# Kernel tuning notes

Measured on AMD Instinct MI355X. Metric: run time of the kernel, lower is better.

Reference implementation:

```python
import jax, jax.numpy as jnp
import numpy as np

B, S, HID = 1, 2048, 2048
NH, NKV, D = 32, 4, 128   # query heads, kv heads, head_dim
ROPE_THETA = 1e6
EPS = 1e-6


def _rms_norm(x, w):
    # per-head RMSNorm over head_dim, computed in fp32 (Qwen3MoeRMSNorm)
    xf = x.astype(jnp.float32)
    var = jnp.mean(xf * xf, axis=-1, keepdims=True)
    return (w * (xf * jax.lax.rsqrt(var + EPS))).astype(x.dtype)


def _rotate_half(x):
    x1, x2 = jnp.split(x, 2, axis=-1)
    return jnp.concatenate([-x2, x1], axis=-1)


def setup_inputs() -> dict:
    key = jax.random.key(0)
    ks = jax.random.split(key, 5)
    hidden_states = jax.random.normal(ks[0], (B, S, HID), jnp.float32)
    # weights stored as (in, out); torch Linear computes x @ W.T with W (out,in) -- same math
    wq = jax.random.normal(ks[1], (HID, NH * D), jnp.float32) * 0.02
    wk = jax.random.normal(ks[2], (HID, NKV * D), jnp.float32) * 0.02
    wv = jax.random.normal(ks[3], (HID, NKV * D), jnp.float32) * 0.02
    wo = jax.random.normal(ks[4], (NH * D, HID), jnp.float32) * 0.02
    q_norm_w = jnp.ones((D,), jnp.float32)
    k_norm_w = jnp.ones((D,), jnp.float32)
    # RoPE tables (rotate_half convention, like HF Qwen3)
    inv_freq = 1.0 / (ROPE_THETA ** (jnp.arange(0, D, 2, dtype=jnp.float32) / D))
    freqs = jnp.arange(S, dtype=jnp.float32)[:, None] * inv_freq[None, :]  # [S, D/2]
    emb = jnp.concatenate([freqs, freqs], axis=-1)  # [S, D]
    cos, sin = jnp.cos(emb), jnp.sin(emb)
    # causal mask (True = keep)
    attention_mask = jnp.tril(jnp.ones((S, S), bool))[None, None]
    return {
        'hidden_states': hidden_states, 'cos': cos, 'sin': sin,
        'wq': wq, 'wk': wk, 'wv': wv, 'wo': wo,
        'q_norm_w': q_norm_w, 'k_norm_w': k_norm_w,
        'attention_mask': attention_mask, 'start_pos': 0,
    }


def reference(hidden_states, cos, sin, wq, wk, wv, wo, q_norm_w, k_norm_w,
              attention_mask, start_pos):
    b, s, _ = hidden_states.shape
    # projections + per-head RMSNorm, then [B, H, S, D]
    q = _rms_norm((hidden_states @ wq).reshape(b, s, NH, D), q_norm_w).transpose(0, 2, 1, 3)
    k = _rms_norm((hidden_states @ wk).reshape(b, s, NKV, D), k_norm_w).transpose(0, 2, 1, 3)
    v = (hidden_states @ wv).reshape(b, s, NKV, D).transpose(0, 2, 1, 3)
    # rotary embedding (rotate_half form); start_pos=0 -> tables already aligned
    c = cos[None, None, :, :]
    sn = sin[None, None, :, :]
    q = q * c + _rotate_half(q) * sn
    k = k * c + _rotate_half(k) * sn
    # GQA: repeat kv heads to match query heads
    groups = NH // NKV
    k = jnp.repeat(k, groups, axis=1)
    v = jnp.repeat(v, groups, axis=1)
    scaling = D ** -0.5
    scores = jnp.einsum('bhqd,bhkd->bhqk', q, k) * scaling  # [B, NH, S, S]
    scores = jnp.where(attention_mask, scores, jnp.float32(-1e9))
    attn = jax.nn.softmax(scores, axis=-1)
    out = jnp.einsum('bhqk,bhkd->bhqd', attn, v)  # [B, NH, S, D]
    out = out.transpose(0, 2, 1, 3).reshape(b, s, NH * D)
    return out @ wo
```

## Files before the change

kernel.cpp:

```cpp
#include <hip/hip_runtime.h>
#include <hip/hip_bf16.h>

using short4v = __attribute__((ext_vector_type(4))) short;
using short8 = __attribute__((ext_vector_type(8))) short;
using f32x4  = __attribute__((ext_vector_type(4))) float;

#define SEQ 2048
#define NHEAD 32
#define NKVH 4
#define HDIM 128
#define QK_SCALE_LOG2 (0.08838834764831845f * 1.44269504088896340f)

__device__ __forceinline__ float fast_exp2(float x) { return __builtin_amdgcn_exp2f(x); }
__device__ __forceinline__ float b2f(short u) {
    return __uint_as_float(((unsigned)(unsigned short)u) << 16);
}
__device__ __forceinline__ short f2bb(float f) {
    __hip_bfloat16 h = __float2bfloat16(f);
    return *reinterpret_cast<short*>(&h);
}

__global__ __launch_bounds__(256) void prep_kernel(
    const float* __restrict__ hs, __hip_bfloat16* __restrict__ hsb,
    const float* __restrict__ wq, const float* __restrict__ wk, const float* __restrict__ wv,
    const float* __restrict__ wo,
    __hip_bfloat16* __restrict__ WqkvT, __hip_bfloat16* __restrict__ WoT) {
    const int b = blockIdx.x, tid = threadIdx.x;
    if (b < 4096) {
        int i = b * 256 + tid;
        float4 v = ((const float4*)hs)[i];
        __hip_bfloat16 h4[4] = {__float2bfloat16(v.x), __float2bfloat16(v.y),
                                __float2bfloat16(v.z), __float2bfloat16(v.w)};
        ((ushort4*)hsb)[i] = *(ushort4*)h4;
        return;
    }
    __shared__ float tile[32][33];
    const float* W; __hip_bfloat16* Wt; int N, ld, nb, kb;
    if (b < 12288)      { int bb = b - 4096;  W = wq; Wt = WqkvT;                       N = 4096; ld = 2048; nb = (bb & 127) * 32; kb = (bb >> 7) * 32; }
    else if (b < 13312) { int bb = b - 12288; W = wk; Wt = WqkvT + (size_t)4096 * 2048; N = 512;  ld = 2048; nb = (bb & 15) * 32;  kb = (bb >> 4) * 32; }
    else if (b < 14336) { int bb = b - 13312; W = wv; Wt = WqkvT + (size_t)4608 * 2048; N = 512;  ld = 2048; nb = (bb & 15) * 32;  kb = (bb >> 4) * 32; }
    else                { int bb = b - 14336; W = wo; Wt = WoT;                         N = 2048; ld = 4096; nb = (bb & 63) * 32;  kb = (bb >> 6) * 32; }
    int tx = tid & 31, ty = tid >> 5;
    for (int j = 0; j < 32; j += 8)
        tile[ty + j][tx] = W[(size_t)(kb + ty + j) * N + nb + tx];
    __syncthreads();
    for (int j = 0; j < 32; j += 8)
        Wt[(size_t)(nb + ty + j) * ld + kb + tx] = __float2bfloat16(tile[tx][ty + j]);
}

__global__ void add3b_kernel(const __hip_bfloat16* __restrict__ a, const __hip_bfloat16* __restrict__ b,
                             const __hip_bfloat16* __restrict__ c, float* __restrict__ o, int n4) {
    int i = blockIdx.x * blockDim.x + threadIdx.x;
    if (i >= n4) return;
    short4v x = ((const short4v*)a)[i];
    short4v y = ((const short4v*)b)[i];
    short4v z = ((const short4v*)c)[i];
    float4 r = {b2f(x[0]) + b2f(y[0]) + b2f(z[0]), b2f(x[1]) + b2f(y[1]) + b2f(z[1]),
                b2f(x[2]) + b2f(y[2]) + b2f(z[2]), b2f(x[3]) + b2f(y[3]) + b2f(z[3])};
    ((float4*)o)[i] = r;
}

#define BM 128
#define BN 128
#define BKK 32
template <typename OutT>
__global__ __launch_bounds__(256) void gemm_bt_kernel(
    const __hip_bfloat16* __restrict__ A, const __hip_bfloat16* __restrict__ Bt,
    OutT* __restrict__ C, int M, int N, int KextMax, int ld, int koff, long long czstride, int Ktot) {
    const int kstart = blockIdx.z * koff;
    const int Kext = min(KextMax, Ktot - kstart);
    A  += (size_t)kstart;
    Bt += (size_t)kstart;
    C  += (size_t)blockIdx.z * czstride;
    __shared__ __align__(16) __hip_bfloat16 sA[BM * BKK];
    __shared__ __align__(16) __hip_bfloat16 sB[BN * BKK];
    const int tid = threadIdx.x;
    const int w = tid >> 6, l = tid & 63;
    const int wr = w >> 1, wc = w & 1;
    const int row0 = blockIdx.y * BM;
    const int col0 = blockIdx.x * BN;
    const int srow = l >> 2;
    const int scol = (l & 3) * 8;

    f32x4 acc[4][4] = {};
    const int fr = l & 15;
    const int fc = (l >> 4) * 8;

    for (int k0 = 0; k0 < Kext; k0 += BKK) {
        for (int i = 0; i < 2; ++i) {
            int c = i * 4 + w;
            const __hip_bfloat16* ga = A + (size_t)(row0 + c * 16 + srow) * ld + k0 + scol;
            __builtin_amdgcn_global_load_lds((const __attribute__((address_space(1))) void*)ga,
                                             (__attribute__((address_space(3))) void*)&sA[c * 16 * BKK], 16, 0, 0);
            const __hip_bfloat16* gb = Bt + (size_t)(col0 + c * 16 + srow) * ld + k0 + scol;
            __builtin_amdgcn_global_load_lds((const __attribute__((address_space(1))) void*)gb,
                                             (__attribute__((address_space(3))) void*)&sB[c * 16 * BKK], 16, 0, 0);
        }
        __syncthreads();
        short8 af[4], bfr[4];
        for (int m = 0; m < 4; ++m)
            af[m] = *(const short8*)&sA[(wr * 64 + m * 16 + fr) * BKK + fc];
        for (int n = 0; n < 4; ++n)
            bfr[n] = *(const short8*)&sB[(wc * 64 + n * 16 + fr) * BKK + fc];
        for (int m = 0; m < 4; ++m)
            for (int n = 0; n < 4; ++n)
                acc[m][n] = __builtin_amdgcn_mfma_f32_16x16x32_bf16(af[m], bfr[n], acc[m][n], 0, 0, 0);
        __syncthreads();
    }
    const int fq = l >> 4;
    for (int m = 0; m < 4; ++m)
        for (int n = 0; n < 4; ++n)
            for (int r = 0; r < 4; ++r) {
                int row = row0 + wr * 64 + m * 16 + fq * 4 + r;
                int col = col0 + wc * 64 + n * 16 + fr;
                float v = acc[m][n][r];
                if constexpr (__is_same(OutT, float)) C[(size_t)row * N + col] = v;
                else C[(size_t)row * N + col] = __float2bfloat16(v);
            }
}

__global__ __launch_bounds__(256) void pack_kernel(
    const __hip_bfloat16* __restrict__ P0, const __hip_bfloat16* __restrict__ P1,
    const float* __restrict__ cosp, const float* __restrict__ sinp,
    const float* __restrict__ qnw, const float* __restrict__ knw,
    __hip_bfloat16* __restrict__ Qh, __hip_bfloat16* __restrict__ Kh, __hip_bfloat16* __restrict__ Vt) {
    const int tid = threadIdx.x;
    const int rloc = tid >> 4, l16 = tid & 15;
    const int r = blockIdx.y * 16 + rloc;
    const int s = blockIdx.x * 2 + (r >= 40 ? 1 : 0);
    const int slot = (r >= 40) ? r - 40 : r;
    int off;
    if (slot < 32)      off = slot * 128;
    else if (slot < 36) off = 4096 + (slot - 32) * 128;
    else                off = 4608 + (slot - 36) * 128;
    const int d0 = l16 * 4;
    const size_t base = (size_t)s * 5120 + off;

    short4v a0 = *(const short4v*)&P0[base + d0];
    short4v a1 = *(const short4v*)&P0[base + d0 + 64];
    short4v b0 = *(const short4v*)&P1[base + d0];
    short4v b1 = *(const short4v*)&P1[base + d0 + 64];
    float x1[4], x2[4];
    for (int j = 0; j < 4; ++j) {
        x1[j] = b2f(a0[j]) + b2f(b0[j]);
        x2[j] = b2f(a1[j]) + b2f(b1[j]);
    }

    if (slot >= 36) {
        int t = slot - 36;
        for (int j = 0; j < 4; ++j) {
            Vt[((size_t)t * 128 + d0 + j) * SEQ + s]      = __float2bfloat16(x1[j]);
            Vt[((size_t)t * 128 + d0 + 64 + j) * SEQ + s] = __float2bfloat16(x2[j]);
        }
        return;
    }
    float ss = 0.f;
    for (int j = 0; j < 4; ++j) ss += x1[j] * x1[j] + x2[j] * x2[j];
    for (int x = 1; x < 16; x <<= 1) ss += __shfl_xor(ss, x);
    float rs = rsqrtf(ss * (1.0f / 128.0f) + 1e-6f);

    f32x4 c4 = *(const f32x4*)&cosp[(size_t)s * 128 + d0];
    f32x4 s4 = *(const f32x4*)&sinp[(size_t)s * 128 + d0];
    const float* wgt = (slot < 32) ? qnw : knw;
    f32x4 w1 = *(const f32x4*)&wgt[d0];
    f32x4 w2 = *(const f32x4*)&wgt[d0 + 64];
    const float scl = (slot < 32) ? QK_SCALE_LOG2 : 1.0f;

    short4v o1, o2;
    for (int j = 0; j < 4; ++j) {
        float a = x1[j] * rs * w1[j], b = x2[j] * rs * w2[j];
        o1[j] = f2bb((a * c4[j] - b * s4[j]) * scl);
        o2[j] = f2bb((b * c4[j] + a * s4[j]) * scl);
    }
    __hip_bfloat16* dst;
    if (slot < 32) dst = Qh + ((size_t)slot * SEQ + s) * 128;
    else           dst = Kh + ((size_t)(slot - 32) * SEQ + s) * 128;
    *(short4v*)&dst[d0]      = o1;
    *(short4v*)&dst[d0 + 64] = o2;
}

__global__ __launch_bounds__(256, 2) void attn_kernel(
    const __hip_bfloat16* __restrict__ Qh,
    const __hip_bfloat16* __restrict__ Kh,
    const __hip_bfloat16* __restrict__ Vt,
    __hip_bfloat16* __restrict__ Oa) {
    __shared__ __align__(16) __hip_bfloat16 sK[2][64 * 128];
    __shared__ __align__(16) __hip_bfloat16 sV[2][128 * 64];
    __shared__ __align__(16) __hip_bfloat16 sP[4][16 * 72];

    const int tid = threadIdx.x;
    const int w = tid >> 6, l = tid & 63;
    const int bx = blockIdx.x;
    const int y = bx & 7;
    const int qtA = bx >> 3;
    const int qbaseA = qtA * 16;
    const int qbaseB = (127 - qtA) * 16;
    const int hkv = y >> 1;
    const int h = y * 4 + w;
    const int fr = l & 15, g = l >> 4;

    const __hip_bfloat16* Kp = Kh + (size_t)hkv * SEQ * HDIM;
    const __hip_bfloat16* Vp = Vt + (size_t)hkv * HDIM * SEQ;
    __hip_bfloat16* myP = &sP[w][0];

    short8 qfA[4], qfB[4];
    {
        const __hip_bfloat16* QpA = Qh + ((size_t)h * SEQ + qbaseA) * HDIM;
        const __hip_bfloat16* QpB = Qh + ((size_t)h * SEQ + qbaseB) * HDIM;
        for (int c = 0; c < 4; ++c) {
            qfA[c] = *(const short8*)&QpA[fr * HDIM + c * 32 + g * 8];
            qfB[c] = *(const short8*)&QpB[fr * HDIM + c * 32 + g * 8];
        }
    }

    f32x4 oaccA[8] = {}, oaccB[8] = {};
    float mrowA[4], lpartA[4], mrowB[4], lpartB[4];
    for (int r = 0; r < 4; ++r) {
        mrowA[r] = -3.0e38f; lpartA[r] = 0.f;
        mrowB[r] = -3.0e38f; lpartB[r] = 0.f;
    }

    const int xr = (fr & 7) << 4;
    const int nA = ((qbaseA + 15) >> 6) + 1;
    const int nB = ((qbaseB + 15) >> 6) + 1;

    auto stage = [&](int buf, int kbase) {
        for (int i = 0; i < 4; ++i) {
            int blk = i * 4 + w;
            {
                int row = blk * 4 + (l >> 4);
                int cb = ((l & 15) * 16) ^ ((row & 7) << 4);
                const __hip_bfloat16* src = Kp + (size_t)(kbase + row) * HDIM + (cb >> 1);
                __builtin_amdgcn_global_load_lds((const __attribute__((address_space(1))) void*)src,
                    (__attribute__((address_space(3))) void*)&sK[buf][blk * 512], 16, 0, 0);
            }
            {
                int row = blk * 8 + (l >> 3);
                int cb = ((l & 7) * 16) ^ ((row & 7) << 4);
                const __hip_bfloat16* src = Vp + (size_t)row * SEQ + kbase + (cb >> 1);
                __builtin_amdgcn_global_load_lds((const __attribute__((address_space(1))) void*)src,
                    (__attribute__((address_space(3))) void*)&sV[buf][blk * 512], 16, 0, 0);
            }
        }
    };

#define PROCESS(QF, OACC, MROW, LPART, QBASE)                                          \
    {                                                                                  \
        f32x4 s[4] = {};                                                               \
        __builtin_amdgcn_s_setprio(1);                                                 \
        for (int j = 0; j < 4; ++j) {                                                  \
            const __hip_bfloat16* kp = &sK[buf][(j * 16 + fr) * 128];                  \
            for (int c = 0; c < 4; ++c) {                                              \
                short8 kf = *(const short8*)&kp[((c * 64 + g * 16) ^ xr) >> 1];        \
                s[j] = __builtin_amdgcn_mfma_f32_16x16x32_bf16(QF[c], kf, s[j], 0, 0, 0); \
            }                                                                          \
        }                                                                              \
        __builtin_amdgcn_s_setprio(0);                                                 \
        float v[4][4], mloc[4];                                                        \
        const bool full = (kbase + 63 <= (QBASE));                                     \
        for (int r = 0; r < 4; ++r) {                                                  \
            if (full) {                                                                \
                v[r][0] = s[0][r]; v[r][1] = s[1][r]; v[r][2] = s[2][r]; v[r][3] = s[3][r]; \
            } else {                                                                   \
                const int qg = (QBASE) + g * 4 + r;                                    \
                v[r][0] = (kbase + fr      <= qg) ? s[0][r] : -1e30f;                  \
                v[r][1] = (kbase + 16 + fr <= qg) ? s[1][r] : -1e30f;                  \
                v[r][2] = (kbase + 32 + fr <= qg) ? s[2][r] : -1e30f;                  \
                v[r][3] = (kbase + 48 + fr <= qg) ? s[3][r] : -1e30f;                  \
            }                                                                          \
            float m = fmaxf(fmaxf(v[r][0], v[r][1]), fmaxf(v[r][2], v[r][3]));         \
            for (int x = 1; x < 16; x <<= 1) m = fmaxf(m, __shfl_xor(m, x));           \
            mloc[r] = m;                                                               \
        }                                                                              \
        int grow = (mloc[0] > MROW[0] + 12.0f) | (mloc[1] > MROW[1] + 12.0f) |         \
                   (mloc[2] > MROW[2] + 12.0f) | (mloc[3] > MROW[3] + 12.0f);          \
        if (__any(grow)) {                                                             \
            for (int r = 0; r < 4; ++r) {                                              \
                float mnew = fmaxf(MROW[r], mloc[r]);                                  \
                float corr = fast_exp2(MROW[r] - mnew);                                \
                MROW[r] = mnew;                                                        \
                LPART[r] *= corr;                                                      \
                for (int dt = 0; dt < 8; ++dt) OACC[dt][r] *= corr;                    \
            }                                                                          \
        }                                                                              \
        for (int r = 0; r < 4; ++r) {                                                  \
            float e0 = fast_exp2(v[r][0] - MROW[r]);                                   \
            float e1 = fast_exp2(v[r][1] - MROW[r]);                                   \
            float e2 = fast_exp2(v[r][2] - MROW[r]);                                   \
            float e3 = fast_exp2(v[r][3] - MROW[r]);                                   \
            LPART[r] += (e0 + e1) + (e2 + e3);                                         \
            const int prow = (g * 4 + r) * 72;                                         \
            myP[prow + fr]      = __float2bfloat16(e0);                                \
            myP[prow + 16 + fr] = __float2bfloat16(e1);                                \
            myP[prow + 32 + fr] = __float2bfloat16(e2);                                \
            myP[prow + 48 + fr] = __float2bfloat16(e3);                                \
        }                                                                              \
        short8 pa0 = *(const short8*)&myP[fr * 72 + g * 8];                            \
        short8 pa1 = *(const short8*)&myP[fr * 72 + 32 + g * 8];                       \
        __builtin_amdgcn_s_setprio(1);                                                 \
        for (int dt = 0; dt < 8; ++dt) {                                               \
            const __hip_bfloat16* vp = &sV[buf][(dt * 16 + fr) * 64];                  \
            short8 vb0 = *(const short8*)&vp[((g * 16)      ^ xr) >> 1];               \
            short8 vb1 = *(const short8*)&vp[((g * 16 + 64) ^ xr) >> 1];               \
            OACC[dt] = __builtin_amdgcn_mfma_f32_16x16x32_bf16(pa0, vb0, OACC[dt], 0, 0, 0); \
            OACC[dt] = __builtin_amdgcn_mfma_f32_16x16x32_bf16(pa1, vb1, OACC[dt], 0, 0, 0); \
        }                                                                              \
        __builtin_amdgcn_s_setprio(0);                                                 \
    }

    stage(0, 0);
    __syncthreads();

    for (int t = 0; t < nB; ++t) {
        const int kbase = t * 64;
        const int buf = t & 1;
        if (t + 1 < nB) stage(buf ^ 1, kbase + 64);

        if (t < nA) PROCESS(qfA, oaccA, mrowA, lpartA, qbaseA);
        PROCESS(qfB, oaccB, mrowB, lpartB, qbaseB);

        __syncthreads();
    }
#undef PROCESS

    float invA[4], invB[4];
    for (int r = 0; r < 4; ++r) {
        float la = lpartA[r], lb = lpartB[r];
        for (int x = 1; x < 16; x <<= 1) { la += __shfl_xor(la, x); lb += __shfl_xor(lb, x); }
        invA[r] = 1.0f / la;
        invB[r] = 1.0f / lb;
    }
    for (int dt = 0; dt < 8; ++dt)
        for (int r = 0; r < 4; ++r) {
            int qgA = qbaseA + g * 4 + r;
            int qgB = qbaseB + g * 4 + r;
            Oa[(size_t)qgA * (NHEAD * HDIM) + h * HDIM + dt * 16 + fr] =
                __float2bfloat16(oaccA[dt][r] * invA[r]);
            Oa[(size_t)qgB * (NHEAD * HDIM) + h * HDIM + dt * 16 + fr] =
                __float2bfloat16(oaccB[dt][r] * invB[r]);
        }
}

extern "C" void kernel_launch(void* const* d_in, const int* in_sizes, int n_in,
                              void* d_out, int out_size, void* d_ws, size_t ws_size,
                              hipStream_t stream) {
    const float* hs   = (const float*)d_in[0];
    const float* cosp = (const float*)d_in[1];
    const float* sinp = (const float*)d_in[2];
    const float* wq   = (const float*)d_in[3];
    const float* wk   = (const float*)d_in[4];
    const float* wv   = (const float*)d_in[5];
    const float* wo   = (const float*)d_in[6];
    const float* qnw  = (const float*)d_in[7];
    const float* knw  = (const float*)d_in[8];
    float* out = (float*)d_out;
    char* ws = (char*)d_ws;

    __hip_bfloat16* hsb    = (__hip_bfloat16*)(ws);
    __hip_bfloat16* WqkvT  = (__hip_bfloat16*)(ws + 8388608);
    __hip_bfloat16* WoT    = (__hip_bfloat16*)(ws + 29360128);
    __hip_bfloat16* P0     = (__hip_bfloat16*)(ws + 46137344);
    __hip_bfloat16* P1     = (__hip_bfloat16*)(ws + 67108864);
    __hip_bfloat16* Qh     = (__hip_bfloat16*)(ws + 8388608);
    __hip_bfloat16* Kh     = (__hip_bfloat16*)(ws + 25165824);
    __hip_bfloat16* Vt     = (__hip_bfloat16*)(ws + 27262976);
    __hip_bfloat16* Oa     = (__hip_bfloat16*)(ws + 46137344);
    __hip_bfloat16* Qb     = (__hip_bfloat16*)(ws);

    prep_kernel<<<22528, 256, 0, stream>>>(hs, hsb, wq, wk, wv, wo, WqkvT, WoT);
    gemm_bt_kernel<__hip_bfloat16><<<dim3(40, 16, 2), 256, 0, stream>>>(
        hsb, WqkvT, P0, 2048, 5120, 1024, 2048, 1024, 10485760LL, 2048);
    pack_kernel<<<dim3(1024, 5), 256, 0, stream>>>(P0, P1, cosp, sinp, qnw, knw, Qh, Kh, Vt);
    attn_kernel<<<dim3(512), 256, 0, stream>>>(Qh, Kh, Vt, Oa);
    gemm_bt_kernel<__hip_bfloat16><<<dim3(16, 16, 3), 256, 0, stream>>>(
        Oa, WoT, Qb, 2048, 2048, 1376, 4096, 1376, 4194304LL, 4096);
    add3b_kernel<<<4096, 256, 0, stream>>>(Qb, Qb + 4194304, Qb + 8388608, out, (2048 * 2048) / 4);
}
```

Before: 241.2 us.

## Widen GEMM K-tile to 64 with swizzled LDS and transpose attention score MFMA

The GEMM now stages 64-wide K tiles with an XOR-swizzled LDS layout, halving barrier count per K and avoiding bank conflicts on fragment reads. The attention kernel swaps MFMA operands so each lane owns one query row, which collapses the per-row max/sum shuffle reductions to two cross-group shuffles and lets P be written as packed short4 stores. The output-projection split-K chunk is changed from 1376 to 1408 to stay a multiple of the new 64 K-tile. This adds LDS usage per GEMM block and more correction shuffles on rescale.

```diff
diff --git a/kernel.cpp b/kernel.cpp
--- a/kernel.cpp
+++ b/kernel.cpp
@@ -18,6 +18,10 @@
 __device__ __forceinline__ short f2bb(float f) {
     __hip_bfloat16 h = __float2bfloat16(f);
     return *reinterpret_cast<short*>(&h);
+}
+__device__ __forceinline__ void gload_lds16(const __hip_bfloat16* src, __hip_bfloat16* dst) {
+    __builtin_amdgcn_global_load_lds((const __attribute__((address_space(1))) void*)src,
+                                     (__attribute__((address_space(3))) void*)dst, 16, 0, 0);
 }
 
 __global__ __launch_bounds__(256) void prep_kernel(
@@ -62,7 +66,7 @@
 
 #define BM 128
 #define BN 128
-#define BKK 32
+#define BK2 64
 template <typename OutT>
 __global__ __launch_bounds__(256) void gemm_bt_kernel(
     const __hip_bfloat16* __restrict__ A, const __hip_bfloat16* __restrict__ Bt,
@@ -72,42 +76,45 @@
     A  += (size_t)kstart;
     Bt += (size_t)kstart;
     C  += (size_t)blockIdx.z * czstride;
-    __shared__ __align__(16) __hip_bfloat16 sA[BM * BKK];
-    __shared__ __align__(16) __hip_bfloat16 sB[BN * BKK];
+    __shared__ __align__(16) __hip_bfloat16 sA[BM * BK2];
+    __shared__ __align__(16) __hip_bfloat16 sB[BN * BK2];
     const int tid = threadIdx.x;
     const int w = tid >> 6, l = tid & 63;
     const int wr = w >> 1, wc = w & 1;
     const int row0 = blockIdx.y * BM;
     const int col0 = blockIdx.x * BN;
-    const int srow = l >> 2;
-    const int scol = (l & 3) * 8;
+    const int fr = l & 15;
+    const int fq = l >> 4;
+    const int xs = (fr & 7) << 4;
 
     f32x4 acc[4][4] = {};
-    const int fr = l & 15;
-    const int fc = (l >> 4) * 8;
-
-    for (int k0 = 0; k0 < Kext; k0 += BKK) {
-        for (int i = 0; i < 2; ++i) {
-            int c = i * 4 + w;
-            const __hip_bfloat16* ga = A + (size_t)(row0 + c * 16 + srow) * ld + k0 + scol;
-            __builtin_amdgcn_global_load_lds((const __attribute__((address_space(1))) void*)ga,
-                                             (__attribute__((address_space(3))) void*)&sA[c * 16 * BKK], 16, 0, 0);
-            const __hip_bfloat16* gb = Bt + (size_t)(col0 + c * 16 + srow) * ld + k0 + scol;
-            __builtin_amdgcn_global_load_lds((const __attribute__((address_space(1))) void*)gb,
-                                             (__attribute__((address_space(3))) void*)&sB[c * 16 * BKK], 16, 0, 0);
+
+    for (int k0 = 0; k0 < Kext; k0 += BK2) {
+        for (int i = 0; i < 4; ++i) {
+            int ch = i * 256 + tid;
+            int row = ch >> 3;
+            int cb = ((ch & 7) * 16) ^ ((row & 7) << 4);
+            gload_lds16(A  + (size_t)(row0 + row) * ld + k0 + (cb >> 1), &sA[ch * 8]);
+            gload_lds16(Bt + (size_t)(col0 + row) * ld + k0 + (cb >> 1), &sB[ch * 8]);
         }
         __syncthreads();
-        short8 af[4], bfr[4];
-        for (int m = 0; m < 4; ++m)
-            af[m] = *(const short8*)&sA[(wr * 64 + m * 16 + fr) * BKK + fc];
-        for (int n = 0; n < 4; ++n)
-            bfr[n] = *(const short8*)&sB[(wc * 64 + n * 16 + fr) * BKK + fc];
-        for (int m = 0; m < 4; ++m)
-            for (int n = 0; n < 4; ++n)
-                acc[m][n] = __builtin_amdgcn_mfma_f32_16x16x32_bf16(af[m], bfr[n], acc[m][n], 0, 0, 0);
+        short8 af[4][2], bfr[4][2];
+        for (int m = 0; m < 4; ++m) {
+            const char* base = (const char*)sA + (wr * 64 + m * 16 + fr) * 128;
+            af[m][0] = *(const short8*)(base + (((fq) * 16)     ^ xs));
+            af[m][1] = *(const short8*)(base + (((fq + 4) * 16) ^ xs));
+        }
+        for (int n = 0; n < 4; ++n) {
+            const char* base = (const char*)sB + (wc * 64 + n * 16 + fr) * 128;
+            bfr[n][0] = *(const short8*)(base + (((fq) * 16)     ^ xs));
+            bfr[n][1] = *(const short8*)(base + (((fq + 4) * 16) ^ xs));
+        }
+        for (int kk = 0; kk < 2; ++kk)
+            for (int m = 0; m < 4; ++m)
+                for (int n = 0; n < 4; ++n)
+                    acc[m][n] = __builtin_amdgcn_mfma_f32_16x16x32_bf16(af[m][kk], bfr[n][kk], acc[m][n], 0, 0, 0);
         __syncthreads();
     }
-    const int fq = l >> 4;
     for (int m = 0; m < 4; ++m)
         for (int n = 0; n < 4; ++n)
             for (int r = 0; r < 4; ++r) {
@@ -201,7 +208,7 @@
 
     const __hip_bfloat16* Kp = Kh + (size_t)hkv * SEQ * HDIM;
     const __hip_bfloat16* Vp = Vt + (size_t)hkv * HDIM * SEQ;
-    __hip_bfloat16* myP = &sP[w][0];
+    char* myP = (char*)&sP[w][0];
 
     short8 qfA[4], qfB[4];
     {
@@ -214,13 +221,12 @@
     }
 
     f32x4 oaccA[8] = {}, oaccB[8] = {};
-    float mrowA[4], lpartA[4], mrowB[4], lpartB[4];
-    for (int r = 0; r < 4; ++r) {
-        mrowA[r] = -3.0e38f; lpartA[r] = 0.f;
-        mrowB[r] = -3.0e38f; lpartB[r] = 0.f;
-    }
+    float msA = -3.0e38f, lsA = 0.f;
+    float msB = -3.0e38f, lsB = 0.f;
 
     const int xr = (fr & 7) << 4;
+    const int qgA = qbaseA + fr;
+    const int qgB = qbaseB + fr;
     const int nA = ((qbaseA + 15) >> 6) + 1;
     const int nB = ((qbaseB + 15) >> 6) + 1;
 
@@ -230,21 +236,17 @@
             {
                 int row = blk * 4 + (l >> 4);
                 int cb = ((l & 15) * 16) ^ ((row & 7) << 4);
-                const __hip_bfloat16* src = Kp + (size_t)(kbase + row) * HDIM + (cb >> 1);
-                __builtin_amdgcn_global_load_lds((const __attribute__((address_space(1))) void*)src,
-                    (__attribute__((address_space(3))) void*)&sK[buf][blk * 512], 16, 0, 0);
+                gload_lds16(Kp + (size_t)(kbase + row) * HDIM + (cb >> 1), &sK[buf][blk * 512]);
             }
             {
                 int row = blk * 8 + (l >> 3);
                 int cb = ((l & 7) * 16) ^ ((row & 7) << 4);
-                const __hip_bfloat16* src = Vp + (size_t)row * SEQ + kbase + (cb >> 1);
-                __builtin_amdgcn_global_load_lds((const __attribute__((address_space(1))) void*)src,
-                    (__attribute__((address_space(3))) void*)&sV[buf][blk * 512], 16, 0, 0);
+                gload_lds16(Vp + (size_t)row * SEQ + kbase + (cb >> 1), &sV[buf][blk * 512]);
             }
         }
     };
 
-#define PROCESS(QF, OACC, MROW, LPART, QBASE)                                          \
+#define PROCESS(QF, OACC, MS, LS, QG, QBASE)                                           \
     {                                                                                  \
         f32x4 s[4] = {};                                                               \
         __builtin_amdgcn_s_setprio(1);                                                 \
@@ -252,51 +254,53 @@
             const __hip_bfloat16* kp = &sK[buf][(j * 16 + fr) * 128];                  \
             for (int c = 0; c < 4; ++c) {                                              \
                 short8 kf = *(const short8*)&kp[((c * 64 + g * 16) ^ xr) >> 1];        \
-                s[j] = __builtin_amdgcn_mfma_f32_16x16x32_bf16(QF[c], kf, s[j], 0, 0, 0); \
+                s[j] = __builtin_amdgcn_mfma_f32_16x16x32_bf16(kf, QF[c], s[j], 0, 0, 0); \
             }                                                                          \
         }                                                                              \
         __builtin_amdgcn_s_setprio(0);                                                 \
-        float v[4][4], mloc[4];                                                        \
+        float v[4][4];                                                                 \
         const bool full = (kbase + 63 <= (QBASE));                                     \
-        for (int r = 0; r < 4; ++r) {                                                  \
-            if (full) {                                                                \
-                v[r][0] = s[0][r]; v[r][1] = s[1][r]; v[r][2] = s[2][r]; v[r][3] = s[3][r]; \
-            } else {                                                                   \
-                const int qg = (QBASE) + g * 4 + r;                                    \
-                v[r][0] = (kbase + fr      <= qg) ? s[0][r] : -1e30f;                  \
-                v[r][1] = (kbase + 16 + fr <= qg) ? s[1][r] : -1e30f;                  \
-                v[r][2] = (kbase + 32 + fr <= qg) ? s[2][r] : -1e30f;                  \
-                v[r][3] = (kbase + 48 + fr <= qg) ? s[3][r] : -1e30f;                  \
+        if (full) {                                                                    \
+            for (int j = 0; j < 4; ++j)                                                \
+                for (int r = 0; r < 4; ++r) v[j][r] = s[j][r];                         \
+        } else {                                                                       \
+            const int kb0 = kbase + g * 4;                                             \
+            for (int j = 0; j < 4; ++j)                                                \
+                for (int r = 0; r < 4; ++r)                                            \
+                    v[j][r] = (kb0 + j * 16 + r <= (QG)) ? s[j][r] : -1e30f;           \
+        }                                                                              \
+        float m0 = fmaxf(fmaxf(v[0][0], v[0][1]), fmaxf(v[0][2], v[0][3]));            \
+        float m1 = fmaxf(fmaxf(v[1][0], v[1][1]), fmaxf(v[1][2], v[1][3]));            \
+        float m2 = fmaxf(fmaxf(v[2][0], v[2][1]), fmaxf(v[2][2], v[2][3]));            \
+        float m3 = fmaxf(fmaxf(v[3][0], v[3][1]), fmaxf(v[3][2], v[3][3]));            \
+        float m = fmaxf(fmaxf(m0, m1), fmaxf(m2, m3));                                 \
+        m = fmaxf(m, __shfl_xor(m, 16));                                               \
+        m = fmaxf(m, __shfl_xor(m, 32));                                               \
+        if (__any(m > MS + 12.0f)) {                                                   \
+            float mnew = fmaxf(MS, m);                                                 \
+            float corr = fast_exp2(MS - mnew);                                         \
+            MS = mnew;                                                                 \
+            LS *= corr;                                                                \
+            float c0 = __shfl(corr, g * 4 + 0);                                        \
+            float c1 = __shfl(corr, g * 4 + 1);                                        \
+            float c2 = __shfl(corr, g * 4 + 2);                                        \
+            float c3 = __shfl(corr, g * 4 + 3);                                        \
+            for (int dt = 0; dt < 8; ++dt) {                                           \
+                OACC[dt][0] *= c0; OACC[dt][1] *= c1;                                  \
+                OACC[dt][2] *= c2; OACC[dt][3] *= c3;                                  \
             }                                                                          \
-            float m = fmaxf(fmaxf(v[r][0], v[r][1]), fmaxf(v[r][2], v[r][3]));         \
-            for (int x = 1; x < 16; x <<= 1) m = fmaxf(m, __shfl_xor(m, x));           \
-            mloc[r] = m;                                                               \
-        }                                                                              \
-        int grow = (mloc[0] > MROW[0] + 12.0f) | (mloc[1] > MROW[1] + 12.0f) |         \
-                   (mloc[2] > MROW[2] + 12.0f) | (mloc[3] > MROW[3] + 12.0f);          \
-        if (__any(grow)) {                                                             \
-            for (int r = 0; r < 4; ++r) {                                              \
-                float mnew = fmaxf(MROW[r], mloc[r]);                                  \
-                float corr = fast_exp2(MROW[r] - mnew);                                \
-                MROW[r] = mnew;                                                        \
-                LPART[r] *= corr;                                                      \
-                for (int dt = 0; dt < 8; ++dt) OACC[dt][r] *= corr;                    \
-            }                                                                          \
-        }                                                                              \
-        for (int r = 0; r < 4; ++r) {                                                  \
-            float e0 = fast_exp2(v[r][0] - MROW[r]);                                   \
-            float e1 = fast_exp2(v[r][1] - MROW[r]);                                   \
-            float e2 = fast_exp2(v[r][2] - MROW[r]);                                   \
-            float e3 = fast_exp2(v[r][3] - MROW[r]);                                   \
-            LPART[r] += (e0 + e1) + (e2 + e3);                                         \
-            const int prow = (g * 4 + r) * 72;                                         \
-            myP[prow + fr]      = __float2bfloat16(e0);                                \
-            myP[prow + 16 + fr] = __float2bfloat16(e1);                                \
-            myP[prow + 32 + fr] = __float2bfloat16(e2);                                \
-            myP[prow + 48 + fr] = __float2bfloat16(e3);                                \
-        }                                                                              \
-        short8 pa0 = *(const short8*)&myP[fr * 72 + g * 8];                            \
-        short8 pa1 = *(const short8*)&myP[fr * 72 + 32 + g * 8];                       \
+        }                                                                              \
+        for (int j = 0; j < 4; ++j) {                                                  \
+            float e0 = fast_exp2(v[j][0] - MS);                                        \
+            float e1 = fast_exp2(v[j][1] - MS);                                        \
+            float e2 = fast_exp2(v[j][2] - MS);                                        \
+            float e3 = fast_exp2(v[j][3] - MS);                                        \
+            LS += (e0 + e1) + (e2 + e3);                                               \
+            short4v pw = {f2bb(e0), f2bb(e1), f2bb(e2), f2bb(e3)};                     \
+            *(short4v*)(myP + fr * 144 + j * 32 + g * 8) = pw;                         \
+        }                                                                              \
+        short8 pa0 = *(const short8*)(myP + fr * 144 + g * 16);                        \
+        short8 pa1 = *(const short8*)(myP + fr * 144 + 64 + g * 16);                   \
         __builtin_amdgcn_s_setprio(1);                                                 \
         for (int dt = 0; dt < 8; ++dt) {                                               \
             const __hip_bfloat16* vp = &sV[buf][(dt * 16 + fr) * 64];                  \
@@ -316,27 +320,27 @@
         const int buf = t & 1;
         if (t + 1 < nB) stage(buf ^ 1, kbase + 64);
 
-        if (t < nA) PROCESS(qfA, oaccA, mrowA, lpartA, qbaseA);
-        PROCESS(qfB, oaccB, mrowB, lpartB, qbaseB);
+        if (t < nA) PROCESS(qfA, oaccA, msA, lsA, qgA, qbaseA);
+        PROCESS(qfB, oaccB, msB, lsB, qgB, qbaseB);
 
         __syncthreads();
     }
 #undef PROCESS
 
+    lsA += __shfl_xor(lsA, 16); lsA += __shfl_xor(lsA, 32);
+    lsB += __shfl_xor(lsB, 16); lsB += __shfl_xor(lsB, 32);
     float invA[4], invB[4];
     for (int r = 0; r < 4; ++r) {
-        float la = lpartA[r], lb = lpartB[r];
-        for (int x = 1; x < 16; x <<= 1) { la += __shfl_xor(la, x); lb += __shfl_xor(lb, x); }
-        invA[r] = 1.0f / la;
-        invB[r] = 1.0f / lb;
+        invA[r] = 1.0f / __shfl(lsA, g * 4 + r);
+        invB[r] = 1.0f / __shfl(lsB, g * 4 + r);
     }
     for (int dt = 0; dt < 8; ++dt)
         for (int r = 0; r < 4; ++r) {
-            int qgA = qbaseA + g * 4 + r;
-            int qgB = qbaseB + g * 4 + r;
-            Oa[(size_t)qgA * (NHEAD * HDIM) + h * HDIM + dt * 16 + fr] =
+            int qA = qbaseA + g * 4 + r;
+            int qB = qbaseB + g * 4 + r;
+            Oa[(size_t)qA * (NHEAD * HDIM) + h * HDIM + dt * 16 + fr] =
                 __float2bfloat16(oaccA[dt][r] * invA[r]);
-            Oa[(size_t)qgB * (NHEAD * HDIM) + h * HDIM + dt * 16 + fr] =
+            Oa[(size_t)qB * (NHEAD * HDIM) + h * HDIM + dt * 16 + fr] =
                 __float2bfloat16(oaccB[dt][r] * invB[r]);
         }
 }
@@ -373,6 +377,6 @@
     pack_kernel<<<dim3(1024, 5), 256, 0, stream>>>(P0, P1, cosp, sinp, qnw, knw, Qh, Kh, Vt);
     attn_kernel<<<dim3(512), 256, 0, stream>>>(Qh, Kh, Vt, Oa);
     gemm_bt_kernel<__hip_bfloat16><<<dim3(16, 16, 3), 256, 0, stream>>>(
-        Oa, WoT, Qb, 2048, 2048, 1376, 4096, 1376, 4194304LL, 4096);
+        Oa, WoT, Qb, 2048, 2048, 1408, 4096, 1408, 4194304LL, 4096);
     add3b_kernel<<<4096, 256, 0, stream>>>(Qb, Qb + 4194304, Qb + 8388608, out, (2048 * 2048) / 4);
 }
```

Measured after the change: 209.2 us (median of 3 runs). -13.3%, faster.
